# Optimization experiments

Measured on AMD Instinct MI355X. Metric: run time of the kernel, lower is better.

## Reference

```python
import jax, jax.numpy as jnp
import numpy as np

N = 8192      # nodes
E = 524288    # edges
F_IN = 256
H = 2         # heads
F_OUT = 128   # per-head out channels
LN_EPS = 1e-5
NEG_SLOPE = 0.2


def setup_inputs() -> dict:
    key = jax.random.key(0)
    ks = jax.random.split(key, 12)
    s = 0.05
    inp = {
        "x": jax.random.normal(ks[0], (N, F_IN), jnp.float32),
        "edge_index": jax.random.randint(ks[1], (2, E), 0, N, jnp.int32),
        "W_gat": jax.random.normal(ks[2], (F_IN, H * F_OUT), jnp.float32) * s,
        "att_src": jax.random.normal(ks[3], (H, F_OUT), jnp.float32) * s,
        "att_dst": jax.random.normal(ks[4], (H, F_OUT), jnp.float32) * s,
        "bias_gat": jnp.zeros((H * F_OUT,), jnp.float32),
        "w_a": jax.random.normal(ks[5], (256, 128), jnp.float32) * s,
        "b_a": jnp.zeros((128,), jnp.float32),
        "g_a": jnp.ones((128,), jnp.float32),
        "be_a": jnp.zeros((128,), jnp.float32),
        "w1": jax.random.normal(ks[6], (128, 64), jnp.float32) * s,
        "b1": jnp.zeros((64,), jnp.float32),
        "g1": jnp.ones((64,), jnp.float32),
        "be1": jnp.zeros((64,), jnp.float32),
        "w2": jax.random.normal(ks[7], (64, 32), jnp.float32) * s,
        "b2": jnp.zeros((32,), jnp.float32),
        "g2": jnp.ones((32,), jnp.float32),
        "be2": jnp.zeros((32,), jnp.float32),
        "w3": jax.random.normal(ks[8], (32, 3), jnp.float32) * s,
        "b3": jnp.zeros((3,), jnp.float32),
    }
    return inp


def _layernorm(x, g, b):
    mu = jnp.mean(x, axis=-1, keepdims=True)
    var = jnp.mean(jnp.square(x - mu), axis=-1, keepdims=True)
    return (x - mu) * jax.lax.rsqrt(var + LN_EPS) * g + b


def _gat_conv(x, edge_index, W, a_src, a_dst, bias):
    # PyG GATConv with add_self_loops=True, concat=True, dropout=0
    loop = jnp.arange(N, dtype=edge_index.dtype)
    src = jnp.concatenate([edge_index[0], loop])  # [E+N]
    dst = jnp.concatenate([edge_index[1], loop])
    h = (x @ W).reshape(N, H, F_OUT)              # per-node transform
    a_s = jnp.sum(h * a_src, axis=-1)             # [N,H]
    a_d = jnp.sum(h * a_dst, axis=-1)             # [N,H]
    e = jax.nn.leaky_relu(a_s[src] + a_d[dst], NEG_SLOPE)  # [E+N,H]
    # segment softmax over incoming edges of each dst node
    emax = jax.ops.segment_max(e, dst, num_segments=N)
    ex = jnp.exp(e - emax[dst])
    denom = jax.ops.segment_sum(ex, dst, num_segments=N)
    alpha = ex / (denom[dst] + 1e-16)             # [E+N,H]
    msg = h[src] * alpha[:, :, None]              # [E+N,H,F_OUT]
    out = jax.ops.segment_sum(msg, dst, num_segments=N)
    return out.reshape(N, H * F_OUT) + bias


def _safe_cdist(z):
    sq = jnp.sum(z * z, axis=-1)                  # [N]
    d2 = sq[:, None] + sq[None, :] - 2.0 * (z @ z.T)
    d2 = jnp.maximum(d2, 0.0)
    pos = d2 > 0
    return jnp.where(pos, jnp.sqrt(jnp.where(pos, d2, 1.0)), 0.0)


def reference(x, edge_index, W_gat, att_src, att_dst, bias_gat,
              w_a, b_a, g_a, be_a, w1, b1, g1, be1,
              w2, b2, g2, be2, w3, b3):
    h = _gat_conv(x, edge_index, W_gat, att_src, att_dst, bias_gat)
    h = jax.nn.relu(h)
    h = jax.nn.relu(_layernorm(h @ w_a + b_a, g_a, be_a))
    h = jax.nn.relu(_layernorm(h @ w1 + b1, g1, be1))
    h = jax.nn.relu(_layernorm(h @ w2 + b2, g2, be2))
    h = h @ w3 + b3                               # [N,3]
    return _safe_cdist(h)                         # [N,N]
```

## Files before the change

kernel.cpp:

```cpp
#include <hip/hip_runtime.h>
#include <hip/hip_bf16.h>

#define N_NODES 8192
#define E_EDGES 524288
#define F_IN    256
#define NH      2
#define F_OUT   128
#define C0      256
#define E_TOT   (E_EDGES + N_NODES)

typedef float f32x4 __attribute__((ext_vector_type(4)));
typedef _Float16 f16x4 __attribute__((ext_vector_type(4)));

__global__ __launch_bounds__(256) void gemm_xw_k(const float* __restrict__ A,
                                                 const float* __restrict__ B,
                                                 float* __restrict__ C) {
  const int K = 256, NC = 256;
  __shared__ float As[16][68];
  __shared__ float Bs[16][68];
  int bm = blockIdx.y * 64;
  int bn = blockIdx.x * 64;
  int tid = threadIdx.x;
  int tm = (tid >> 4) << 2;
  int tn = (tid & 15) << 2;
  float acc[4][4] = {};
  for (int k0 = 0; k0 < K; k0 += 16) {
#pragma unroll
    for (int i = 0; i < 4; i++) {
      int idx = tid + i * 256;
      int m = idx >> 4, k = idx & 15;
      As[k][m] = A[(bm + m) * K + k0 + k];
    }
#pragma unroll
    for (int i = 0; i < 4; i++) {
      int idx = tid + i * 256;
      int k = idx >> 6, n = idx & 63;
      Bs[k][n] = B[(k0 + k) * NC + bn + n];
    }
    __syncthreads();
#pragma unroll
    for (int k = 0; k < 16; k++) {
      float4 a = *(const float4*)&As[k][tm];
      float4 b = *(const float4*)&Bs[k][tn];
      acc[0][0] += a.x * b.x; acc[0][1] += a.x * b.y; acc[0][2] += a.x * b.z; acc[0][3] += a.x * b.w;
      acc[1][0] += a.y * b.x; acc[1][1] += a.y * b.y; acc[1][2] += a.y * b.z; acc[1][3] += a.y * b.w;
      acc[2][0] += a.z * b.x; acc[2][1] += a.z * b.y; acc[2][2] += a.z * b.z; acc[2][3] += a.z * b.w;
      acc[3][0] += a.w * b.x; acc[3][1] += a.w * b.y; acc[3][2] += a.w * b.z; acc[3][3] += a.w * b.w;
    }
    __syncthreads();
  }
#pragma unroll
  for (int i = 0; i < 4; i++) {
    float4 o = {acc[i][0], acc[i][1], acc[i][2], acc[i][3]};
    *(float4*)&C[(bm + tm + i) * NC + bn + tn] = o;
  }
}

__global__ __launch_bounds__(256) void att_scores_k(const float* __restrict__ h,
                                                    const float* __restrict__ att_src,
                                                    const float* __restrict__ att_dst,
                                                    float* __restrict__ a_s,
                                                    float* __restrict__ a_d,
                                                    _Float16* __restrict__ h16) {
  int wave = threadIdx.x >> 6;
  int lane = threadIdx.x & 63;
  int node = blockIdx.x * 4 + wave;
  if (node >= N_NODES) return;
  const float4 hv = *(const float4*)(h + (size_t)node * C0 + lane * 4);
  f16x4 hh;
  hh.x = (_Float16)hv.x; hh.y = (_Float16)hv.y;
  hh.z = (_Float16)hv.z; hh.w = (_Float16)hv.w;
  *(f16x4*)(h16 + (size_t)node * C0 + lane * 4) = hh;
  const float4 vs = *(const float4*)(att_src + lane * 4);
  const float4 vd = *(const float4*)(att_dst + lane * 4);
  float s = hv.x * vs.x + hv.y * vs.y + hv.z * vs.z + hv.w * vs.w;
  float d = hv.x * vd.x + hv.y * vd.y + hv.z * vd.z + hv.w * vd.w;
#pragma unroll
  for (int off = 16; off; off >>= 1) {
    s += __shfl_xor(s, off);
    d += __shfl_xor(d, off);
  }
  if (lane == 0)  { a_s[node * 2] = s;     a_d[node * 2] = d; }
  if (lane == 32) { a_s[node * 2 + 1] = s; a_d[node * 2 + 1] = d; }
}

__global__ __launch_bounds__(256) void hist_k(const int* __restrict__ ei,
                                              int* __restrict__ deg) {
  int e = blockIdx.x * 256 + threadIdx.x;
  if (e < E_EDGES) atomicAdd(&deg[ei[E_EDGES + e]], 1);
}

__global__ __launch_bounds__(256) void scan_k(const int* __restrict__ deg,
                                              int* __restrict__ offs,
                                              int* __restrict__ cursor) {
  __shared__ int sums[256];
  int t = threadIdx.x;
  int local[32];
  int s = 0;
#pragma unroll
  for (int i = 0; i < 32; i++) { local[i] = s; s += deg[t * 32 + i] + 1; }
  sums[t] = s;
  __syncthreads();
  for (int off = 1; off < 256; off <<= 1) {
    int u = (t >= off) ? sums[t - off] : 0;
    __syncthreads();
    if (t >= off) sums[t] += u;
    __syncthreads();
  }
  int base = sums[t] - s;
#pragma unroll
  for (int i = 0; i < 32; i++) {
    int o = base + local[i];
    offs[t * 32 + i] = o;
    cursor[t * 32 + i] = o;
  }
  if (t == 255) offs[N_NODES] = sums[255];
}

__global__ __launch_bounds__(256) void scatter_k(const int* __restrict__ ei,
                                                 const float* __restrict__ a_s,
                                                 const float* __restrict__ a_d,
                                                 int* __restrict__ cursor,
                                                 int* __restrict__ sorted_src,
                                                 float2* __restrict__ exv) {
  int e = blockIdx.x * 256 + threadIdx.x;
  if (e >= E_TOT) return;
  int s, d;
  if (e < E_EDGES) { s = ei[e]; d = ei[E_EDGES + e]; }
  else             { s = d = e - E_EDGES; }
  const float2 as = ((const float2*)a_s)[s];
  const float2 ad = ((const float2*)a_d)[d];
  float v0 = as.x + ad.x; v0 = v0 > 0.0f ? v0 : 0.2f * v0;
  float v1 = as.y + ad.y; v1 = v1 > 0.0f ? v1 : 0.2f * v1;
  int p = atomicAdd(&cursor[d], 1);
  sorted_src[p] = s;
  exv[p] = make_float2(__expf(v0), __expf(v1));
}

__global__ __launch_bounds__(256) void gat_gather_k(const int* __restrict__ sorted_src,
                                                    const float2* __restrict__ exv,
                                                    const int* __restrict__ offs,
                                                    const _Float16* __restrict__ h16,
                                                    float* __restrict__ gat) {
  int wave = threadIdx.x >> 6;
  int lane = threadIdx.x & 63;
  int node = blockIdx.x * 4 + wave;
  if (node >= N_NODES) return;
  int start = __builtin_amdgcn_readfirstlane(offs[node]);
  int end   = __builtin_amdgcn_readfirstlane(offs[node + 1]);
  int head = lane >> 5;
  float4 acc = {0, 0, 0, 0};
  float den = 0.0f;
  int e = start;
  for (; e + 4 <= end; e += 4) {
    int s0 = sorted_src[e];
    int s1 = sorted_src[e + 1];
    int s2 = sorted_src[e + 2];
    int s3 = sorted_src[e + 3];
    float2 x0 = exv[e];
    float2 x1 = exv[e + 1];
    float2 x2 = exv[e + 2];
    float2 x3 = exv[e + 3];
    f16x4 hv0 = *(const f16x4*)(h16 + (size_t)s0 * C0 + lane * 4);
    f16x4 hv1 = *(const f16x4*)(h16 + (size_t)s1 * C0 + lane * 4);
    f16x4 hv2 = *(const f16x4*)(h16 + (size_t)s2 * C0 + lane * 4);
    f16x4 hv3 = *(const f16x4*)(h16 + (size_t)s3 * C0 + lane * 4);
    float w0 = head ? x0.y : x0.x;
    float w1 = head ? x1.y : x1.x;
    float w2 = head ? x2.y : x2.x;
    float w3 = head ? x3.y : x3.x;
    den += (w0 + w1) + (w2 + w3);
    acc.x = fmaf((float)hv0.x, w0, acc.x); acc.y = fmaf((float)hv0.y, w0, acc.y);
    acc.z = fmaf((float)hv0.z, w0, acc.z); acc.w = fmaf((float)hv0.w, w0, acc.w);
    acc.x = fmaf((float)hv1.x, w1, acc.x); acc.y = fmaf((float)hv1.y, w1, acc.y);
    acc.z = fmaf((float)hv1.z, w1, acc.z); acc.w = fmaf((float)hv1.w, w1, acc.w);
    acc.x = fmaf((float)hv2.x, w2, acc.x); acc.y = fmaf((float)hv2.y, w2, acc.y);
    acc.z = fmaf((float)hv2.z, w2, acc.z); acc.w = fmaf((float)hv2.w, w2, acc.w);
    acc.x = fmaf((float)hv3.x, w3, acc.x); acc.y = fmaf((float)hv3.y, w3, acc.y);
    acc.z = fmaf((float)hv3.z, w3, acc.z); acc.w = fmaf((float)hv3.w, w3, acc.w);
  }
  for (; e < end; e++) {
    int s0 = sorted_src[e];
    float2 x0 = exv[e];
    f16x4 hv0 = *(const f16x4*)(h16 + (size_t)s0 * C0 + lane * 4);
    float w0 = head ? x0.y : x0.x;
    den += w0;
    acc.x = fmaf((float)hv0.x, w0, acc.x); acc.y = fmaf((float)hv0.y, w0, acc.y);
    acc.z = fmaf((float)hv0.z, w0, acc.z); acc.w = fmaf((float)hv0.w, w0, acc.w);
  }
  float inv = 1.0f / (den + 1e-16f);
  float4 o = {acc.x * inv, acc.y * inv, acc.z * inv, acc.w * inv};
  *(float4*)(gat + (size_t)node * C0 + lane * 4) = o;
}

template <int KDIM, int ODIM, bool APPLY_IN, bool FUSE_Z>
__global__ __launch_bounds__(256) void fused_layer_k(const float* __restrict__ in,
                                                     const float* __restrict__ bias_in,
                                                     const float* __restrict__ W,
                                                     const float* __restrict__ b,
                                                     const float* __restrict__ g,
                                                     const float* __restrict__ be,
                                                     float* __restrict__ out,
                                                     const float* __restrict__ w3,
                                                     const float* __restrict__ b3,
                                                     float* __restrict__ zout) {
  const int TILE = 16;
  const int GROUPS = 256 / ODIM;
  const int NPT = TILE / GROUPS;
  __shared__ float in_t[TILE][KDIM + 4];
  __shared__ float out_t[TILE][ODIM + 1];
  int tid = threadIdx.x;
  int n0 = blockIdx.x * TILE;
  const int KD4 = KDIM / 4;
  for (int idx = tid; idx < TILE * KD4; idx += 256) {
    int n = idx / KD4, k4 = idx % KD4;
    float4 v = *(const float4*)&in[(size_t)(n0 + n) * KDIM + k4 * 4];
    if (APPLY_IN) {
      const float4 bb = *(const float4*)&bias_in[k4 * 4];
      v.x = fmaxf(v.x + bb.x, 0.0f);
      v.y = fmaxf(v.y + bb.y, 0.0f);
      v.z = fmaxf(v.z + bb.z, 0.0f);
      v.w = fmaxf(v.w + bb.w, 0.0f);
    }
    *(float4*)&in_t[n][k4 * 4] = v;
  }
  __syncthreads();
  int jj = tid % ODIM;
  int grp = tid / ODIM;
  float acc[NPT];
#pragma unroll
  for (int t = 0; t < NPT; t++) acc[t] = b[jj];
  for (int k = 0; k < KDIM; k += 4) {
    float w0 = W[(k + 0) * ODIM + jj];
    float w1 = W[(k + 1) * ODIM + jj];
    float w2 = W[(k + 2) * ODIM + jj];
    float w3v = W[(k + 3) * ODIM + jj];
#pragma unroll
    for (int t = 0; t < NPT; t++) {
      float4 v = *(const float4*)&in_t[grp + t * GROUPS][k];
      acc[t] = fmaf(v.w, w3v, fmaf(v.z, w2, fmaf(v.y, w1, fmaf(v.x, w0, acc[t]))));
    }
  }
#pragma unroll
  for (int t = 0; t < NPT; t++) out_t[grp + t * GROUPS][jj] = acc[t];
  __syncthreads();
  const int TPN = 256 / TILE;
  const int JPT = ODIM / TPN;
  int node = tid / TPN;
  int ln = tid % TPN;
  float v[JPT];
  float s = 0;
#pragma unroll
  for (int q = 0; q < JPT; q++) { v[q] = out_t[node][ln + q * TPN]; s += v[q]; }
#pragma unroll
  for (int m = 1; m < TPN; m <<= 1) s += __shfl_xor(s, m);
  float mu = s / (float)ODIM;
  float vs = 0;
#pragma unroll
  for (int q = 0; q < JPT; q++) { float dd = v[q] - mu; vs += dd * dd; }
#pragma unroll
  for (int m = 1; m < TPN; m <<= 1) vs += __shfl_xor(vs, m);
  float inv = rsqrtf(vs / (float)ODIM + 1e-5f);
  if (FUSE_Z) {
    float p0 = 0, p1 = 0, p2 = 0;
#pragma unroll
    for (int q = 0; q < JPT; q++) {
      int j = ln + q * TPN;
      float val = fmaxf((v[q] - mu) * inv * g[j] + be[j], 0.0f);
      p0 = fmaf(val, w3[j * 3 + 0], p0);
      p1 = fmaf(val, w3[j * 3 + 1], p1);
      p2 = fmaf(val, w3[j * 3 + 2], p2);
    }
#pragma unroll
    for (int m = 1; m < TPN; m <<= 1) {
      p0 += __shfl_xor(p0, m);
      p1 += __shfl_xor(p1, m);
      p2 += __shfl_xor(p2, m);
    }
    if (ln == 0) {
      float4 zz = {p0 + b3[0], p1 + b3[1], p2 + b3[2], 0.0f};
      ((float4*)zout)[n0 + node] = zz;
    }
  } else {
#pragma unroll
    for (int q = 0; q < JPT; q++) {
      int j = ln + q * TPN;
      float o = (v[q] - mu) * inv * g[j] + be[j];
      out[(size_t)(n0 + node) * ODIM + j] = fmaxf(o, 0.0f);
    }
  }
}

__global__ __launch_bounds__(256) void cdist_k(const float* __restrict__ z,
                                               float* __restrict__ out) {
  int i = blockIdx.x >> 3;
  int j0 = (((blockIdx.x & 7) << 8) + threadIdx.x) << 2;
  const float4 zi = ((const float4*)z)[i];
  f32x4 r;
  {
    float4 zj = ((const float4*)z)[j0 + 0];
    float dx = zi.x - zj.x, dy = zi.y - zj.y, dz = zi.z - zj.z;
    r.x = sqrtf(dx * dx + dy * dy + dz * dz);
  }
  {
    float4 zj = ((const float4*)z)[j0 + 1];
    float dx = zi.x - zj.x, dy = zi.y - zj.y, dz = zi.z - zj.z;
    r.y = sqrtf(dx * dx + dy * dy + dz * dz);
  }
  {
    float4 zj = ((const float4*)z)[j0 + 2];
    float dx = zi.x - zj.x, dy = zi.y - zj.y, dz = zi.z - zj.z;
    r.z = sqrtf(dx * dx + dy * dy + dz * dz);
  }
  {
    float4 zj = ((const float4*)z)[j0 + 3];
    float dx = zi.x - zj.x, dy = zi.y - zj.y, dz = zi.z - zj.z;
    r.w = sqrtf(dx * dx + dy * dy + dz * dz);
  }
  f32x4* dst = (f32x4*)out + (((size_t)i * N_NODES + j0) >> 2);
  __builtin_nontemporal_store(r, dst);
}

extern "C" void kernel_launch(void* const* d_in, const int* in_sizes, int n_in,
                              void* d_out, int out_size, void* d_ws, size_t ws_size,
                              hipStream_t stream) {
  const float* x        = (const float*)d_in[0];
  const int*   ei       = (const int*)d_in[1];
  const float* W_gat    = (const float*)d_in[2];
  const float* att_src  = (const float*)d_in[3];
  const float* att_dst  = (const float*)d_in[4];
  const float* bias_gat = (const float*)d_in[5];
  const float* w_a      = (const float*)d_in[6];
  const float* b_a      = (const float*)d_in[7];
  const float* g_a      = (const float*)d_in[8];
  const float* be_a     = (const float*)d_in[9];
  const float* w1       = (const float*)d_in[10];
  const float* b1       = (const float*)d_in[11];
  const float* g1       = (const float*)d_in[12];
  const float* be1      = (const float*)d_in[13];
  const float* w2       = (const float*)d_in[14];
  const float* b2       = (const float*)d_in[15];
  const float* g2       = (const float*)d_in[16];
  const float* be2      = (const float*)d_in[17];
  const float* w3       = (const float*)d_in[18];
  const float* b3       = (const float*)d_in[19];
  float* out = (float*)d_out;

  float* ws = (float*)d_ws;
  float*    h      = ws;
  float*    a_s    = h + 2097152;
  float*    a_d    = a_s + 16384;
  float*    gat    = a_d + 16384;
  float*    hA     = gat + 2097152;
  float*    h1     = hA + 1048576;
  float*    z      = h1 + 524288;
  float2*   exv    = (float2*)(z + 32768);
  _Float16* h16    = (_Float16*)((float*)(exv + E_TOT));
  int*      deg    = (int*)((float*)h16 + 1048576);
  int*      offs   = deg + 8192;
  int*      cursor = offs + 8200;
  int*      sorted = cursor + 8192;

  hipMemsetAsync(deg, 0, N_NODES * sizeof(int), stream);

  gemm_xw_k<<<dim3(4, 128), 256, 0, stream>>>(x, W_gat, h);
  att_scores_k<<<2048, 256, 0, stream>>>(h, att_src, att_dst, a_s, a_d, h16);
  hist_k<<<E_EDGES / 256, 256, 0, stream>>>(ei, deg);
  scan_k<<<1, 256, 0, stream>>>(deg, offs, cursor);
  scatter_k<<<E_TOT / 256, 256, 0, stream>>>(ei, a_s, a_d, cursor, sorted, exv);
  gat_gather_k<<<2048, 256, 0, stream>>>(sorted, exv, offs, h16, gat);
  fused_layer_k<256, 128, true,  false><<<N_NODES / 16, 256, 0, stream>>>(gat, bias_gat, w_a, b_a, g_a, be_a, hA, nullptr, nullptr, nullptr);
  fused_layer_k<128, 64,  false, false><<<N_NODES / 16, 256, 0, stream>>>(hA, nullptr, w1, b1, g1, be1, h1, nullptr, nullptr, nullptr);
  fused_layer_k<64,  32,  false, true ><<<N_NODES / 16, 256, 0, stream>>>(h1, nullptr, w2, b2, g2, be2, nullptr, w3, b3, z);
  cdist_k<<<N_NODES * 8, 256, 0, stream>>>(z, out);
}
```

Measured before the change: 461.9 us.

## Fuse attention scores into XW GEMM epilogue and merge MLP layers into one kernel

The GEMM epilogue now writes fp16 h directly and computes per-head attention score partials, reducing across the 64-column tile with shuffles and atomics. This removes the fp32 h buffer and the separate att_scores kernel. The three MLP layer kernels are merged into a single kernel that keeps intermediates in shared memory, which avoids global round trips for hA and h1 and two launches. In exchange, a_s and a_d must be zeroed via memset, float atomics make the score summation order nondeterministic, and the merged kernel's larger shared memory footprint may lower occupancy.

```diff
diff --git a/kernel.cpp b/kernel.cpp
--- a/kernel.cpp
+++ b/kernel.cpp
@@ -14,7 +14,11 @@
 
 __global__ __launch_bounds__(256) void gemm_xw_k(const float* __restrict__ A,
                                                  const float* __restrict__ B,
-                                                 float* __restrict__ C) {
+                                                 const float* __restrict__ att_src,
+                                                 const float* __restrict__ att_dst,
+                                                 _Float16* __restrict__ h16,
+                                                 float* __restrict__ a_s,
+                                                 float* __restrict__ a_d) {
   const int K = 256, NC = 256;
   __shared__ float As[16][68];
   __shared__ float Bs[16][68];
@@ -49,39 +53,25 @@
     }
     __syncthreads();
   }
+  int head = bn >> 7;
+  const float4 asv = *(const float4*)(att_src + bn + tn);
+  const float4 adv = *(const float4*)(att_dst + bn + tn);
 #pragma unroll
   for (int i = 0; i < 4; i++) {
-    float4 o = {acc[i][0], acc[i][1], acc[i][2], acc[i][3]};
-    *(float4*)&C[(bm + tm + i) * NC + bn + tn] = o;
-  }
-}
-
-__global__ __launch_bounds__(256) void att_scores_k(const float* __restrict__ h,
-                                                    const float* __restrict__ att_src,
-                                                    const float* __restrict__ att_dst,
-                                                    float* __restrict__ a_s,
-                                                    float* __restrict__ a_d,
-                                                    _Float16* __restrict__ h16) {
-  int wave = threadIdx.x >> 6;
-  int lane = threadIdx.x & 63;
-  int node = blockIdx.x * 4 + wave;
-  if (node >= N_NODES) return;
-  const float4 hv = *(const float4*)(h + (size_t)node * C0 + lane * 4);
-  f16x4 hh;
-  hh.x = (_Float16)hv.x; hh.y = (_Float16)hv.y;
-  hh.z = (_Float16)hv.z; hh.w = (_Float16)hv.w;
-  *(f16x4*)(h16 + (size_t)node * C0 + lane * 4) = hh;
-  const float4 vs = *(const float4*)(att_src + lane * 4);
-  const float4 vd = *(const float4*)(att_dst + lane * 4);
-  float s = hv.x * vs.x + hv.y * vs.y + hv.z * vs.z + hv.w * vs.w;
-  float d = hv.x * vd.x + hv.y * vd.y + hv.z * vd.z + hv.w * vd.w;
-#pragma unroll
-  for (int off = 16; off; off >>= 1) {
-    s += __shfl_xor(s, off);
-    d += __shfl_xor(d, off);
-  }
-  if (lane == 0)  { a_s[node * 2] = s;     a_d[node * 2] = d; }
-  if (lane == 32) { a_s[node * 2 + 1] = s; a_d[node * 2 + 1] = d; }
+    int row = bm + tm + i;
+    f16x4 hh;
+    hh.x = (_Float16)acc[i][0]; hh.y = (_Float16)acc[i][1];
+    hh.z = (_Float16)acc[i][2]; hh.w = (_Float16)acc[i][3];
+    *(f16x4*)(h16 + (size_t)row * C0 + bn + tn) = hh;
+    float ps = acc[i][0] * asv.x + acc[i][1] * asv.y + acc[i][2] * asv.z + acc[i][3] * asv.w;
+    float pd = acc[i][0] * adv.x + acc[i][1] * adv.y + acc[i][2] * adv.z + acc[i][3] * adv.w;
+#pragma unroll
+    for (int m = 1; m < 16; m <<= 1) { ps += __shfl_xor(ps, m); pd += __shfl_xor(pd, m); }
+    if ((tid & 15) == 0) {
+      atomicAdd(&a_s[row * 2 + head], ps);
+      atomicAdd(&a_d[row * 2 + head], pd);
+    }
+  }
 }
 
 __global__ __launch_bounds__(256) void hist_k(const int* __restrict__ ei,
@@ -193,38 +183,14 @@
   *(float4*)(gat + (size_t)node * C0 + lane * 4) = o;
 }
 
-template <int KDIM, int ODIM, bool APPLY_IN, bool FUSE_Z>
-__global__ __launch_bounds__(256) void fused_layer_k(const float* __restrict__ in,
-                                                     const float* __restrict__ bias_in,
-                                                     const float* __restrict__ W,
-                                                     const float* __restrict__ b,
-                                                     const float* __restrict__ g,
-                                                     const float* __restrict__ be,
-                                                     float* __restrict__ out,
-                                                     const float* __restrict__ w3,
-                                                     const float* __restrict__ b3,
-                                                     float* __restrict__ zout) {
-  const int TILE = 16;
+template <int KDIM, int ODIM>
+__device__ __forceinline__ void layer_gemm(const float (*in_t)[KDIM + 4],
+                                           float (*out_t)[ODIM + 4],
+                                           const float* __restrict__ W,
+                                           const float* __restrict__ b,
+                                           int tid) {
   const int GROUPS = 256 / ODIM;
-  const int NPT = TILE / GROUPS;
-  __shared__ float in_t[TILE][KDIM + 4];
-  __shared__ float out_t[TILE][ODIM + 1];
-  int tid = threadIdx.x;
-  int n0 = blockIdx.x * TILE;
-  const int KD4 = KDIM / 4;
-  for (int idx = tid; idx < TILE * KD4; idx += 256) {
-    int n = idx / KD4, k4 = idx % KD4;
-    float4 v = *(const float4*)&in[(size_t)(n0 + n) * KDIM + k4 * 4];
-    if (APPLY_IN) {
-      const float4 bb = *(const float4*)&bias_in[k4 * 4];
-      v.x = fmaxf(v.x + bb.x, 0.0f);
-      v.y = fmaxf(v.y + bb.y, 0.0f);
-      v.z = fmaxf(v.z + bb.z, 0.0f);
-      v.w = fmaxf(v.w + bb.w, 0.0f);
-    }
-    *(float4*)&in_t[n][k4 * 4] = v;
-  }
-  __syncthreads();
+  const int NPT = 16 / GROUPS;
   int jj = tid % ODIM;
   int grp = tid / ODIM;
   float acc[NPT];
@@ -243,15 +209,21 @@
   }
 #pragma unroll
   for (int t = 0; t < NPT; t++) out_t[grp + t * GROUPS][jj] = acc[t];
-  __syncthreads();
-  const int TPN = 256 / TILE;
+}
+
+template <int ODIM>
+__device__ __forceinline__ void layer_ln_relu(float (*buf)[ODIM + 4],
+                                              const float* __restrict__ g,
+                                              const float* __restrict__ be,
+                                              int tid) {
+  const int TPN = 16;
   const int JPT = ODIM / TPN;
   int node = tid / TPN;
   int ln = tid % TPN;
   float v[JPT];
   float s = 0;
 #pragma unroll
-  for (int q = 0; q < JPT; q++) { v[q] = out_t[node][ln + q * TPN]; s += v[q]; }
+  for (int q = 0; q < JPT; q++) { v[q] = buf[node][ln + q * TPN]; s += v[q]; }
 #pragma unroll
   for (int m = 1; m < TPN; m <<= 1) s += __shfl_xor(s, m);
   float mu = s / (float)ODIM;
@@ -261,12 +233,79 @@
 #pragma unroll
   for (int m = 1; m < TPN; m <<= 1) vs += __shfl_xor(vs, m);
   float inv = rsqrtf(vs / (float)ODIM + 1e-5f);
-  if (FUSE_Z) {
+#pragma unroll
+  for (int q = 0; q < JPT; q++) {
+    int j = ln + q * TPN;
+    buf[node][j] = fmaxf((v[q] - mu) * inv * g[j] + be[j], 0.0f);
+  }
+}
+
+__global__ __launch_bounds__(256) void mlp_all_k(const float* __restrict__ gat,
+                                                 const float* __restrict__ bias_gat,
+                                                 const float* __restrict__ w_a,
+                                                 const float* __restrict__ b_a,
+                                                 const float* __restrict__ g_a,
+                                                 const float* __restrict__ be_a,
+                                                 const float* __restrict__ w1,
+                                                 const float* __restrict__ b1,
+                                                 const float* __restrict__ g1,
+                                                 const float* __restrict__ be1,
+                                                 const float* __restrict__ w2,
+                                                 const float* __restrict__ b2,
+                                                 const float* __restrict__ g2,
+                                                 const float* __restrict__ be2,
+                                                 const float* __restrict__ w3,
+                                                 const float* __restrict__ b3,
+                                                 float* __restrict__ z) {
+  __shared__ float bufA[16][260];
+  __shared__ float bufB[16][132];
+  __shared__ float bufC[16][68];
+  __shared__ float bufD[16][36];
+  int tid = threadIdx.x;
+  int n0 = blockIdx.x * 16;
+  for (int idx = tid; idx < 16 * 64; idx += 256) {
+    int n = idx >> 6, k4 = idx & 63;
+    float4 v = *(const float4*)&gat[(size_t)(n0 + n) * 256 + k4 * 4];
+    const float4 bb = *(const float4*)&bias_gat[k4 * 4];
+    v.x = fmaxf(v.x + bb.x, 0.0f);
+    v.y = fmaxf(v.y + bb.y, 0.0f);
+    v.z = fmaxf(v.z + bb.z, 0.0f);
+    v.w = fmaxf(v.w + bb.w, 0.0f);
+    *(float4*)&bufA[n][k4 * 4] = v;
+  }
+  __syncthreads();
+  layer_gemm<256, 128>(bufA, bufB, w_a, b_a, tid);
+  __syncthreads();
+  layer_ln_relu<128>(bufB, g_a, be_a, tid);
+  __syncthreads();
+  layer_gemm<128, 64>(bufB, bufC, w1, b1, tid);
+  __syncthreads();
+  layer_ln_relu<64>(bufC, g1, be1, tid);
+  __syncthreads();
+  layer_gemm<64, 32>(bufC, bufD, w2, b2, tid);
+  __syncthreads();
+  {
+    const int TPN = 16, JPT = 2;
+    int node = tid / TPN;
+    int ln = tid % TPN;
+    float v[JPT];
+    float s = 0;
+#pragma unroll
+    for (int q = 0; q < JPT; q++) { v[q] = bufD[node][ln + q * TPN]; s += v[q]; }
+#pragma unroll
+    for (int m = 1; m < TPN; m <<= 1) s += __shfl_xor(s, m);
+    float mu = s / 32.0f;
+    float vs = 0;
+#pragma unroll
+    for (int q = 0; q < JPT; q++) { float dd = v[q] - mu; vs += dd * dd; }
+#pragma unroll
+    for (int m = 1; m < TPN; m <<= 1) vs += __shfl_xor(vs, m);
+    float inv = rsqrtf(vs / 32.0f + 1e-5f);
     float p0 = 0, p1 = 0, p2 = 0;
 #pragma unroll
     for (int q = 0; q < JPT; q++) {
       int j = ln + q * TPN;
-      float val = fmaxf((v[q] - mu) * inv * g[j] + be[j], 0.0f);
+      float val = fmaxf((v[q] - mu) * inv * g2[j] + be2[j], 0.0f);
       p0 = fmaf(val, w3[j * 3 + 0], p0);
       p1 = fmaf(val, w3[j * 3 + 1], p1);
       p2 = fmaf(val, w3[j * 3 + 2], p2);
@@ -279,14 +318,7 @@
     }
     if (ln == 0) {
       float4 zz = {p0 + b3[0], p1 + b3[1], p2 + b3[2], 0.0f};
-      ((float4*)zout)[n0 + node] = zz;
-    }
-  } else {
-#pragma unroll
-    for (int q = 0; q < JPT; q++) {
-      int j = ln + q * TPN;
-      float o = (v[q] - mu) * inv * g[j] + be[j];
-      out[(size_t)(n0 + node) * ODIM + j] = fmaxf(o, 0.0f);
+      ((float4*)z)[n0 + node] = zz;
     }
   }
 }
@@ -347,30 +379,25 @@
   float* out = (float*)d_out;
 
   float* ws = (float*)d_ws;
-  float*    h      = ws;
-  float*    a_s    = h + 2097152;
+  float*    a_s    = ws;
   float*    a_d    = a_s + 16384;
-  float*    gat    = a_d + 16384;
-  float*    hA     = gat + 2097152;
-  float*    h1     = hA + 1048576;
-  float*    z      = h1 + 524288;
+  int*      deg    = (int*)(a_d + 16384);
+  _Float16* h16    = (_Float16*)(deg + 8192);
+  float*    gat    = (float*)h16 + 1048576;
+  float*    z      = gat + 2097152;
   float2*   exv    = (float2*)(z + 32768);
-  _Float16* h16    = (_Float16*)((float*)(exv + E_TOT));
-  int*      deg    = (int*)((float*)h16 + 1048576);
-  int*      offs   = deg + 8192;
+  int*      offs   = (int*)(exv + E_TOT);
   int*      cursor = offs + 8200;
   int*      sorted = cursor + 8192;
 
-  hipMemsetAsync(deg, 0, N_NODES * sizeof(int), stream);
-
-  gemm_xw_k<<<dim3(4, 128), 256, 0, stream>>>(x, W_gat, h);
-  att_scores_k<<<2048, 256, 0, stream>>>(h, att_src, att_dst, a_s, a_d, h16);
+  hipMemsetAsync(a_s, 0, (16384 + 16384 + 8192) * sizeof(float), stream);
+
+  gemm_xw_k<<<dim3(4, 128), 256, 0, stream>>>(x, W_gat, att_src, att_dst, h16, a_s, a_d);
   hist_k<<<E_EDGES / 256, 256, 0, stream>>>(ei, deg);
   scan_k<<<1, 256, 0, stream>>>(deg, offs, cursor);
   scatter_k<<<E_TOT / 256, 256, 0, stream>>>(ei, a_s, a_d, cursor, sorted, exv);
   gat_gather_k<<<2048, 256, 0, stream>>>(sorted, exv, offs, h16, gat);
-  fused_layer_k<256, 128, true,  false><<<N_NODES / 16, 256, 0, stream>>>(gat, bias_gat, w_a, b_a, g_a, be_a, hA, nullptr, nullptr, nullptr);
-  fused_layer_k<128, 64,  false, false><<<N_NODES / 16, 256, 0, stream>>>(hA, nullptr, w1, b1, g1, be1, h1, nullptr, nullptr, nullptr);
-  fused_layer_k<64,  32,  false, true ><<<N_NODES / 16, 256, 0, stream>>>(h1, nullptr, w2, b2, g2, be2, nullptr, w3, b3, z);
+  mlp_all_k<<<N_NODES / 16, 256, 0, stream>>>(gat, bias_gat, w_a, b_a, g_a, be_a,
+                                              w1, b1, g1, be1, w2, b2, g2, be2, w3, b3, z);
   cdist_k<<<N_NODES * 8, 256, 0, stream>>>(z, out);
 }
```

Result: no change. 455.5 us (-1.4%).
